# Kernel tuning notes

Hardware: AMD Instinct MI355X
Metric: run time of the kernel (lower is better)

## Reference

```python
import jax, jax.numpy as jnp
import numpy as np

B, S, H = 4, 2048, 768
NH, HD = 12, 64
E, TOPK, F = 8, 2, 3072

def rotate_half(x):
    x1, x2 = x[..., : x.shape[-1] // 2], x[..., x.shape[-1] // 2 :]
    return jnp.concatenate((-x2, x1), axis=-1)

def rope_cache(seq_len, dim, dtype=jnp.float32):
    inv_freq = 1.0 / (10000.0 ** (jnp.arange(0, dim, 2, dtype=jnp.float32) / dim))
    t = jnp.arange(seq_len, dtype=jnp.float32)
    freqs = jnp.einsum('i,j->ij', t, inv_freq)          # [S, dim/2]
    emb = jnp.concatenate((freqs, freqs), axis=-1)       # [S, dim]
    return jnp.cos(emb).astype(dtype), jnp.sin(emb).astype(dtype)

def rmsnorm(x, w):
    eps = jnp.finfo(x.dtype).eps
    var = jnp.mean(jnp.square(x), axis=-1, keepdims=True)
    return x * jax.lax.rsqrt(var + eps) * w

def setup_inputs() -> dict:
    key = jax.random.key(0)
    ks = jax.random.split(key, 9)
    s = lambda fan_in: 1.0 / np.sqrt(fan_in)
    return {
        'x': jax.random.normal(ks[0], (B, S, H), jnp.float32),
        'attention_mask': jnp.ones((B, S), jnp.int32),
        'qkv_w': jax.random.normal(ks[1], (H, 3 * H), jnp.float32) * s(H),
        'out_w': jax.random.normal(ks[2], (H, H), jnp.float32) * s(H),
        'gate_w': jax.random.normal(ks[3], (H, E), jnp.float32) * s(H),
        'w1': jax.random.normal(ks[4], (E, H, F), jnp.float32) * s(H),
        'w2': jax.random.normal(ks[5], (E, F, H), jnp.float32) * s(F),
        'norm1_w': jnp.ones((H,), jnp.float32),
        'norm2_w': jnp.ones((H,), jnp.float32),
    }

def reference(x, attention_mask, qkv_w, out_w, gate_w, w1, w2, norm1_w, norm2_w):
    b, seq, h = x.shape
    # ---- attention with manual RoPE ----
    qkv = (x @ qkv_w).reshape(b, seq, NH, 3 * HD).transpose(0, 2, 1, 3)  # [B,NH,S,3*HD]
    q, k, v = jnp.split(qkv, 3, axis=-1)
    cos, sin = rope_cache(seq, HD, x.dtype)  # [S,HD]
    cos = cos[None, None]; sin = sin[None, None]
    q = q * cos + rotate_half(q) * sin
    k = k * cos + rotate_half(k) * sin
    scores = jnp.einsum('bhqd,bhkd->bhqk', q, k) / jnp.sqrt(jnp.asarray(HD, x.dtype))
    mask = attention_mask[:, None, None, :]  # [B,1,1,S]
    scores = jnp.where(mask == 0, jnp.finfo(scores.dtype).min, scores)
    attn = jax.nn.softmax(scores, axis=-1)
    ctx = jnp.einsum('bhqk,bhkd->bhqd', attn, v)
    ctx = ctx.transpose(0, 2, 1, 3).reshape(b, seq, h)
    attn_out = ctx @ out_w
    x1 = rmsnorm(x + attn_out, norm1_w)
    # ---- MoE ----
    xf = x1.reshape(-1, h)                                # [T,H]
    T = xf.shape[0]
    router_logits = xf @ gate_w                           # [T,E]
    probs = jax.nn.softmax(router_logits.astype(jnp.float32), axis=-1)
    rw, sel = jax.lax.top_k(probs, TOPK)                  # [T,K]
    rw = rw / jnp.sum(rw, axis=-1, keepdims=True)
    # aux load-balancing loss
    counts = jnp.zeros((E,), jnp.float32).at[sel.reshape(-1)].add(1.0)
    f_i = counts / T
    P_i = probs.mean(axis=0)
    aux_loss = E * jnp.sum(f_i * P_i)
    # dense combine weights [T,E] (zero where expert not selected)
    cw = jnp.zeros((T, E), jnp.float32).at[jnp.arange(T)[:, None], sel].add(rw)
    # dense grouped expert compute (same math as gather/index_add dispatch)
    hmid = jax.nn.gelu(jnp.einsum('th,ehf->etf', xf, w1), approximate=False)
    yexp = jnp.einsum('etf,efh->eth', hmid, w2)           # [E,T,H]
    moe_out = jnp.einsum('eth,te->th', yexp, cw.astype(x.dtype))
    x2 = rmsnorm(x1 + moe_out.reshape(b, seq, h), norm2_w)
    return x2, aux_loss
```

## Files before the change

kernel.cpp:

```cpp
#include <hip/hip_runtime.h>
#include <hip/hip_bf16.h>
#include <math.h>

typedef __hip_bfloat16 bf16;
typedef __attribute__((ext_vector_type(8))) short bf16x8;
typedef __attribute__((ext_vector_type(4))) float f32x4;

#define B_ 4
#define S_ 2048
#define H_ 768
#define NH_ 12
#define HD_ 64
#define E_ 8
#define F_ 3072
#define T_ 8192

__device__ __forceinline__ unsigned f2bf(float x){
  unsigned u = __float_as_uint(x);
  return (u + 0x7FFFu + ((u >> 16) & 1u)) >> 16;
}

__device__ __forceinline__ float4 ldA4(const float* p){ return *reinterpret_cast<const float4*>(p); }

__device__ __forceinline__ float block_sum256(float v, float* red){
  int tid = threadIdx.x;
  red[tid] = v; __syncthreads();
  #pragma unroll
  for (int s = 128; s > 0; s >>= 1){
    if (tid < s) red[tid] += red[tid + s];
    __syncthreads();
  }
  float r = red[0];
  __syncthreads();
  return r;
}

__global__ __launch_bounds__(256) void gemm_f32_k(const float* __restrict__ A, const float* __restrict__ Bw,
                                                  float* __restrict__ C, int N, int K)
{
  __shared__ float As[16][132];
  __shared__ float Bs[16][132];
  const int tid = threadIdx.x;
  const int m0 = blockIdx.y * 128, n0 = blockIdx.x * 128;
  const int tm = tid >> 4, tn = tid & 15;
  const int am = tid >> 1, akq = (tid & 1) * 8;
  const int bk = tid >> 4, bnq = (tid & 15) * 8;
  float acc[8][8] = {};
  for (int k0 = 0; k0 < K; k0 += 16){
    float4 a0 = ldA4(&A[(size_t)(m0 + am) * K + k0 + akq]);
    float4 a1 = ldA4(&A[(size_t)(m0 + am) * K + k0 + akq + 4]);
    float4 b0 = ldA4(&Bw[(size_t)(k0 + bk) * N + n0 + bnq]);
    float4 b1 = ldA4(&Bw[(size_t)(k0 + bk) * N + n0 + bnq + 4]);
    As[akq+0][am] = a0.x; As[akq+1][am] = a0.y; As[akq+2][am] = a0.z; As[akq+3][am] = a0.w;
    As[akq+4][am] = a1.x; As[akq+5][am] = a1.y; As[akq+6][am] = a1.z; As[akq+7][am] = a1.w;
    *reinterpret_cast<float4*>(&Bs[bk][bnq])     = b0;
    *reinterpret_cast<float4*>(&Bs[bk][bnq + 4]) = b1;
    __syncthreads();
    #pragma unroll
    for (int kk = 0; kk < 16; ++kk){
      float4 av0 = *reinterpret_cast<const float4*>(&As[kk][tm*8]);
      float4 av1 = *reinterpret_cast<const float4*>(&As[kk][tm*8 + 4]);
      float4 bv0 = *reinterpret_cast<const float4*>(&Bs[kk][tn*8]);
      float4 bv1 = *reinterpret_cast<const float4*>(&Bs[kk][tn*8 + 4]);
      float a[8] = {av0.x,av0.y,av0.z,av0.w,av1.x,av1.y,av1.z,av1.w};
      float b[8] = {bv0.x,bv0.y,bv0.z,bv0.w,bv1.x,bv1.y,bv1.z,bv1.w};
      #pragma unroll
      for (int i = 0; i < 8; ++i)
        #pragma unroll
        for (int j = 0; j < 8; ++j)
          acc[i][j] += a[i]*b[j];
    }
    __syncthreads();
  }
  #pragma unroll
  for (int i = 0; i < 8; ++i){
    int row = m0 + tm*8 + i;
    float* dst = &C[(size_t)row * N + n0 + tn*8];
    *reinterpret_cast<float4*>(dst)     = make_float4(acc[i][0], acc[i][1], acc[i][2], acc[i][3]);
    *reinterpret_cast<float4*>(dst + 4) = make_float4(acc[i][4], acc[i][5], acc[i][6], acc[i][7]);
  }
}

__global__ __launch_bounds__(256) void rope_k(float* __restrict__ qkv)
{
  int idx = blockIdx.x * 256 + threadIdx.x;
  int j  = idx & 31;
  int hh = (idx >> 5) % NH_;
  int t  = idx / (32 * NH_);
  int s  = t & (S_ - 1);
  double invf = pow(10000.0, -(double)j / 32.0);
  float ph = (float)((double)s * invf);
  float sn, cs;
  sincosf(ph, &sn, &cs);
  float* base = qkv + (size_t)t * 2304 + hh * 192;
  float q0 = base[j],    q1 = base[32+j];
  base[j]    = q0*cs - q1*sn;
  base[32+j] = q1*cs + q0*sn;
  float k0 = base[64+j], k1 = base[96+j];
  base[64+j] = k0*cs - k1*sn;
  base[96+j] = k1*cs + k0*sn;
}

__global__ __launch_bounds__(256) void attn_mfma_k(const float* __restrict__ qkv,
                                                   const int* __restrict__ amask,
                                                   float* __restrict__ ctx)
{
  __shared__ __align__(16) short Kl[64*72];
  __shared__ __align__(16) short Vt[64*72];
  __shared__ __align__(16) short Pl[64*72];
  const int tid = threadIdx.x;
  const int qt = blockIdx.x & 31;
  const int hh = (blockIdx.x >> 5) % NH_;
  const int b  = blockIdx.x / (32 * NH_);
  const size_t tb = (size_t)b * S_;
  const int q0 = qt * 64;
  const int lane = tid & 63, w = tid >> 6;
  const int quad = lane >> 4, l15 = lane & 15;
  const int swl = (l15 & 12) << 1;

  bf16x8 qf[2];
  {
    const float* qrow = qkv + (tb + q0 + w*16 + l15) * 2304 + hh*192;
    #pragma unroll
    for (int ks = 0; ks < 2; ++ks){
      float4 f0 = ldA4(qrow + ks*32 + quad*8);
      float4 f1 = ldA4(qrow + ks*32 + quad*8 + 4);
      union { bf16x8 v; unsigned u[4]; } u;
      u.u[0] = f2bf(f0.x*0.125f) | (f2bf(f0.y*0.125f) << 16);
      u.u[1] = f2bf(f0.z*0.125f) | (f2bf(f0.w*0.125f) << 16);
      u.u[2] = f2bf(f1.x*0.125f) | (f2bf(f1.y*0.125f) << 16);
      u.u[3] = f2bf(f1.z*0.125f) | (f2bf(f1.w*0.125f) << 16);
      qf[ks] = u.v;
    }
  }

  f32x4 O[4];
  #pragma unroll
  for (int i = 0; i < 4; ++i) O[i] = (f32x4){0.f,0.f,0.f,0.f};
  float m_i[4] = {-3.0e38f,-3.0e38f,-3.0e38f,-3.0e38f};
  float l_i[4] = {0.f,0.f,0.f,0.f};

  for (int c = 0; c < 32; ++c){
    __syncthreads();
    #pragma unroll
    for (int i = 0; i < 2; ++i){
      int idx = i*256 + tid;
      int rp = idx >> 4;
      int c4 = (idx & 15) * 4;
      int r = rp * 2;
      const float* src = &qkv[(tb + c*64 + r) * 2304 + hh*192 + 64 + c4];
      float4 k0 = ldA4(src);
      float4 v0 = ldA4(src + 64);
      float4 k1 = ldA4(src + 2304);
      float4 v1 = ldA4(src + 2304 + 64);
      uint2 kw0, kw1;
      kw0.x = f2bf(k0.x) | (f2bf(k0.y) << 16); kw0.y = f2bf(k0.z) | (f2bf(k0.w) << 16);
      kw1.x = f2bf(k1.x) | (f2bf(k1.y) << 16); kw1.y = f2bf(k1.z) | (f2bf(k1.w) << 16);
      *reinterpret_cast<uint2*>(&Kl[ r   *72 + (c4 ^ (( r    & 12) << 1))]) = kw0;
      *reinterpret_cast<uint2*>(&Kl[(r+1)*72 + (c4 ^ (((r+1) & 12) << 1))]) = kw1;
      float vv0[4] = {v0.x,v0.y,v0.z,v0.w};
      float vv1[4] = {v1.x,v1.y,v1.z,v1.w};
      #pragma unroll
      for (int dd = 0; dd < 4; ++dd){
        int d = c4 + dd;
        unsigned pw = f2bf(vv0[dd]) | (f2bf(vv1[dd]) << 16);
        *reinterpret_cast<unsigned*>(&Vt[d*72 + (r ^ ((d & 12) << 1))]) = pw;
      }
    }
    __syncthreads();

    f32x4 sacc[4];
    #pragma unroll
    for (int ni = 0; ni < 4; ++ni) sacc[ni] = (f32x4){0.f,0.f,0.f,0.f};
    #pragma unroll
    for (int ks = 0; ks < 2; ++ks){
      #pragma unroll
      for (int ni = 0; ni < 4; ++ni){
        bf16x8 kf = *reinterpret_cast<const bf16x8*>(
            &Kl[(ni*16 + l15)*72 + ((quad*8 + ks*32) ^ swl)]);
        sacc[ni] = __builtin_amdgcn_mfma_f32_16x16x32_bf16(qf[ks], kf, sacc[ni], 0, 0, 0);
      }
    }

    #pragma unroll
    for (int ni = 0; ni < 4; ++ni){
      int mv = amask[b*S_ + c*64 + ni*16 + l15];
      if (mv == 0){
        sacc[ni][0] = -3.0e38f; sacc[ni][1] = -3.0e38f;
        sacc[ni][2] = -3.0e38f; sacc[ni][3] = -3.0e38f;
      }
    }
    float p[4][4];
    #pragma unroll
    for (int r = 0; r < 4; ++r){
      float v = fmaxf(fmaxf(sacc[0][r], sacc[1][r]), fmaxf(sacc[2][r], sacc[3][r]));
      #pragma unroll
      for (int o = 8; o > 0; o >>= 1) v = fmaxf(v, __shfl_xor(v, o, 64));
      float mn = fmaxf(m_i[r], v);
      float al = __expf(m_i[r] - mn);
      m_i[r] = mn;
      float ts = 0.f;
      #pragma unroll
      for (int ni = 0; ni < 4; ++ni){
        float e = __expf(sacc[ni][r] - mn);
        p[ni][r] = e; ts += e;
      }
      #pragma unroll
      for (int o = 8; o > 0; o >>= 1) ts += __shfl_xor(ts, o, 64);
      l_i[r] = l_i[r]*al + ts;
      #pragma unroll
      for (int nd = 0; nd < 4; ++nd) O[nd][r] *= al;
    }

    #pragma unroll
    for (int ni = 0; ni < 4; ++ni){
      int colp = (ni*16 + l15) ^ (quad << 3);
      #pragma unroll
      for (int r = 0; r < 4; ++r)
        Pl[(w*16 + quad*4 + r)*72 + colp] = (short)f2bf(p[ni][r]);
    }
    bf16x8 pa[2];
    #pragma unroll
    for (int ks = 0; ks < 2; ++ks)
      pa[ks] = *reinterpret_cast<const bf16x8*>(
          &Pl[(w*16 + l15)*72 + ((quad*8 + ks*32) ^ swl)]);

    #pragma unroll
    for (int ks = 0; ks < 2; ++ks){
      #pragma unroll
      for (int nd = 0; nd < 4; ++nd){
        bf16x8 vf = *reinterpret_cast<const bf16x8*>(
            &Vt[(nd*16 + l15)*72 + ((quad*8 + ks*32) ^ swl)]);
        O[nd] = __builtin_amdgcn_mfma_f32_16x16x32_bf16(pa[ks], vf, O[nd], 0, 0, 0);
      }
    }
  }

  #pragma unroll
  for (int r = 0; r < 4; ++r){
    float inv = 1.f / l_i[r];
    int row = q0 + w*16 + quad*4 + r;
    float* dst = &ctx[(tb + row)*H_ + hh*HD_ + l15];
    #pragma unroll
    for (int nd = 0; nd < 4; ++nd)
      dst[nd*16] = O[nd][r] * inv;
  }
}

__global__ __launch_bounds__(256) void norm1_k(const float* __restrict__ x, const float* __restrict__ ao,
                                               const float* __restrict__ w, float* __restrict__ x1)
{
  __shared__ float red[256];
  const int t = blockIdx.x, tid = threadIdx.x;
  float y[3]; float ss = 0.f;
  #pragma unroll
  for (int k = 0; k < 3; ++k){
    int i = tid + k*256;
    y[k] = x[(size_t)t*H_ + i] + ao[(size_t)t*H_ + i];
    ss += y[k]*y[k];
  }
  float tot = block_sum256(ss, red);
  float r = rsqrtf(tot / 768.f + 1.1920928955078125e-07f);
  #pragma unroll
  for (int k = 0; k < 3; ++k){
    int i = tid + k*256;
    x1[(size_t)t*H_ + i] = y[k] * r * w[i];
  }
}

__global__ __launch_bounds__(256) void router_k(const float* __restrict__ x1, const float* __restrict__ gw,
                                                float* __restrict__ rw, int* __restrict__ sel,
                                                float* __restrict__ Psum, int* __restrict__ cnt)
{
  __shared__ float lg[8];
  __shared__ float pr[8];
  const int t = blockIdx.x, tid = threadIdx.x;
  const int e = tid >> 5, l = tid & 31;
  const float* xr = x1 + (size_t)t * H_;
  float p = 0.f;
  for (int k = l; k < H_; k += 32) p += xr[k] * gw[k*E_ + e];
  #pragma unroll
  for (int o = 16; o > 0; o >>= 1) p += __shfl_xor(p, o, 32);
  if (l == 0) lg[e] = p;
  __syncthreads();
  if (tid == 0){
    float m = lg[0];
    #pragma unroll
    for (int i = 1; i < 8; ++i) m = fmaxf(m, lg[i]);
    float pv[8]; float s = 0.f;
    #pragma unroll
    for (int i = 0; i < 8; ++i){ pv[i] = expf(lg[i] - m); s += pv[i]; }
    float invs = 1.f / s;
    #pragma unroll
    for (int i = 0; i < 8; ++i){ pv[i] *= invs; pr[i] = pv[i]; }
    int i0 = 0;
    for (int i = 1; i < 8; ++i) if (pv[i] > pv[i0]) i0 = i;
    int i1 = -1;
    for (int i = 0; i < 8; ++i){ if (i == i0) continue; if (i1 < 0 || pv[i] > pv[i1]) i1 = i; }
    float w0 = pv[i0], w1 = pv[i1], si = 1.f / (w0 + w1);
    rw[2*t] = w0*si; rw[2*t+1] = w1*si;
    sel[2*t] = i0;   sel[2*t+1] = i1;
    atomicAdd(&cnt[i0], 1); atomicAdd(&cnt[i1], 1);
  }
  __syncthreads();
  if (tid < 8) atomicAdd(&Psum[tid], pr[tid]);
}

__global__ void offs_aux_k(const float* __restrict__ Psum, const int* __restrict__ cnt,
                           int* __restrict__ offs, float* __restrict__ aux_out)
{
  __shared__ float red[8];
  const int tid = threadIdx.x;
  if (tid == 0){
    int o = 0;
    for (int e = 0; e < 8; ++e){ offs[e] = o; o += cnt[e]; }
  }
  if (tid < 8) red[tid] = ((float)cnt[tid] / 8192.f) * (Psum[tid] / 8192.f);
  __syncthreads();
  if (tid == 0){
    float s = 0.f;
    for (int e = 0; e < 8; ++e) s += red[e];
    *aux_out = 8.f * s;
  }
}

__global__ __launch_bounds__(256) void scatter_k(const int* __restrict__ sel, const int* __restrict__ offs,
                                                 const float* __restrict__ rw,
                                                 int* __restrict__ cur, int* __restrict__ toka,
                                                 float* __restrict__ wgt)
{
  int t = blockIdx.x*256 + threadIdx.x;
  if (t >= T_) return;
  #pragma unroll
  for (int j = 0; j < 2; ++j){
    int e = sel[2*t + j];
    int pos = atomicAdd(&cur[e], 1);
    int a = offs[e] + pos;
    toka[a] = t;
    wgt[a] = rw[2*t + j];
  }
}

__global__ __launch_bounds__(256) void transpose_conv_k(const float* __restrict__ src,
                                                        unsigned short* __restrict__ dst,
                                                        int R, int C)
{
  __shared__ float T[32][33];
  const float* s = src + (size_t)blockIdx.z * R * C;
  unsigned short* d = dst + (size_t)blockIdx.z * R * C;
  int r0 = blockIdx.y*32, c0 = blockIdx.x*32;
  int t = threadIdx.x;
  int r = t >> 3, c4 = (t & 7) * 4;
  float4 v = ldA4(&s[(size_t)(r0+r)*C + c0 + c4]);
  T[r][c4+0]=v.x; T[r][c4+1]=v.y; T[r][c4+2]=v.z; T[r][c4+3]=v.w;
  __syncthreads();
  int c = t >> 3, r4 = (t & 7) * 4;
  ushort4 o;
  o.x = (unsigned short)f2bf(T[r4+0][c]);
  o.y = (unsigned short)f2bf(T[r4+1][c]);
  o.z = (unsigned short)f2bf(T[r4+2][c]);
  o.w = (unsigned short)f2bf(T[r4+3][c]);
  *reinterpret_cast<ushort4*>(&d[(size_t)(c0+c)*R + r0 + r4]) = o;
}

__global__ __launch_bounds__(256) void moe1_mfma_k(const float* __restrict__ X,
                                                   const unsigned short* __restrict__ Bt,
                                                   const int* __restrict__ offs,
                                                   const int* __restrict__ cnts,
                                                   const int* __restrict__ toka,
                                                   unsigned short* __restrict__ hmid)
{
  const int e = blockIdx.z;
  const int n_e = cnts[e];
  const int mt = blockIdx.y * 128;
  if (mt >= n_e) return;
  const int base = offs[e];
  const unsigned short* Bw = Bt + (size_t)e * (H_*F_);
  __shared__ __align__(16) short Al[8*129*8];
  __shared__ __align__(16) short Bl[8*129*8];
  const int tid = threadIdx.x;
  const int n0 = blockIdx.x * 128;
  int tokm[4];
  #pragma unroll
  for (int i = 0; i < 4; ++i){
    int m = (tid + i*256) >> 3;
    tokm[i] = toka[base + min(mt + m, n_e - 1)];
  }
  const int lane = tid & 63, w = tid >> 6;
  const int wr = w >> 1, wc = w & 1;
  const int quad = lane >> 4, l15 = lane & 15;
  f32x4 acc[4][4];
  #pragma unroll
  for (int a = 0; a < 4; ++a)
    #pragma unroll
    for (int b = 0; b < 4; ++b) acc[a][b] = (f32x4){0.f,0.f,0.f,0.f};

  for (int k0 = 0; k0 < H_; k0 += 64){
    __syncthreads();
    #pragma unroll
    for (int i = 0; i < 4; ++i){
      int c = tid + i*256;
      int m = c >> 3, kc = c & 7;
      const float* src = X + (size_t)tokm[i]*H_ + k0 + kc*8;
      float4 f0 = ldA4(src);
      float4 f1 = ldA4(src + 4);
      int4 pk;
      pk.x = (int)(f2bf(f0.x) | (f2bf(f0.y) << 16));
      pk.y = (int)(f2bf(f0.z) | (f2bf(f0.w) << 16));
      pk.z = (int)(f2bf(f1.x) | (f2bf(f1.y) << 16));
      pk.w = (int)(f2bf(f1.z) | (f2bf(f1.w) << 16));
      *reinterpret_cast<int4*>(&Al[(kc*129 + m)*8]) = pk;
      *reinterpret_cast<int4*>(&Bl[(kc*129 + m)*8]) =
        *reinterpret_cast<const int4*>(&Bw[(size_t)(n0 + m)*H_ + k0 + kc*8]);
    }
    __syncthreads();
    #pragma unroll
    for (int ks = 0; ks < 2; ++ks){
      bf16x8 af[4], bfr[4];
      #pragma unroll
      for (int mi = 0; mi < 4; ++mi)
        af[mi] = *reinterpret_cast<const bf16x8*>(&Al[((ks*4+quad)*129 + wr*64 + mi*16 + l15)*8]);
      #pragma unroll
      for (int ni = 0; ni < 4; ++ni)
        bfr[ni] = *reinterpret_cast<const bf16x8*>(&Bl[((ks*4+quad)*129 + wc*64 + ni*16 + l15)*8]);
      #pragma unroll
      for (int mi = 0; mi < 4; ++mi)
        #pragma unroll
        for (int ni = 0; ni < 4; ++ni)
          acc[mi][ni] = __builtin_amdgcn_mfma_f32_16x16x32_bf16(af[mi], bfr[ni], acc[mi][ni], 0, 0, 0);
    }
  }
  #pragma unroll
  for (int mi = 0; mi < 4; ++mi)
    #pragma unroll
    for (int r = 0; r < 4; ++r){
      int row = mt + wr*64 + mi*16 + quad*4 + r;
      if (row < n_e){
        unsigned short* dst = hmid + (size_t)(base + row)*F_ + n0 + wc*64 + l15;
        #pragma unroll
        for (int ni = 0; ni < 4; ++ni){
          float h = acc[mi][ni][r];
          float g = 0.5f * h * (1.f + erff(h * 0.70710678118654752f));
          dst[ni*16] = (unsigned short)f2bf(g);
        }
      }
    }
}

__global__ __launch_bounds__(256) void moe2_mfma_k(const unsigned short* __restrict__ Hm,
                                                   const unsigned short* __restrict__ Bt,
                                                   const int* __restrict__ offs,
                                                   const int* __restrict__ cnts,
                                                   const int* __restrict__ toka,
                                                   const float* __restrict__ wgt,
                                                   float* __restrict__ x1acc)
{
  const int e = blockIdx.z;
  const int n_e = cnts[e];
  const int mt = blockIdx.y * 128;
  if (mt >= n_e) return;
  const int base = offs[e];
  const unsigned short* Bw = Bt + (size_t)e * (H_*F_);
  __shared__ __align__(16) short Al[8*129*8];
  __shared__ __align__(16) short Bl[8*129*8];
  const int tid = threadIdx.x;
  const int n0 = blockIdx.x * 128;
  const int lane = tid & 63, w = tid >> 6;
  const int wr = w >> 1, wc = w & 1;
  const int quad = lane >> 4, l15 = lane & 15;
  f32x4 acc[4][4];
  #pragma unroll
  for (int a = 0; a < 4; ++a)
    #pragma unroll
    for (int b = 0; b < 4; ++b) acc[a][b] = (f32x4){0.f,0.f,0.f,0.f};

  for (int k0 = 0; k0 < F_; k0 += 64){
    __syncthreads();
    #pragma unroll
    for (int i = 0; i < 4; ++i){
      int c = tid + i*256;
      int m = c >> 3, kc = c & 7;
      int hrow = base + min(mt + m, n_e - 1);
      *reinterpret_cast<int4*>(&Al[(kc*129 + m)*8]) =
        *reinterpret_cast<const int4*>(&Hm[(size_t)hrow*F_ + k0 + kc*8]);
      *reinterpret_cast<int4*>(&Bl[(kc*129 + m)*8]) =
        *reinterpret_cast<const int4*>(&Bw[(size_t)(n0 + m)*F_ + k0 + kc*8]);
    }
    __syncthreads();
    #pragma unroll
    for (int ks = 0; ks < 2; ++ks){
      bf16x8 af[4], bfr[4];
      #pragma unroll
      for (int mi = 0; mi < 4; ++mi)
        af[mi] = *reinterpret_cast<const bf16x8*>(&Al[((ks*4+quad)*129 + wr*64 + mi*16 + l15)*8]);
      #pragma unroll
      for (int ni = 0; ni < 4; ++ni)
        bfr[ni] = *reinterpret_cast<const bf16x8*>(&Bl[((ks*4+quad)*129 + wc*64 + ni*16 + l15)*8]);
      #pragma unroll
      for (int mi = 0; mi < 4; ++mi)
        #pragma unroll
        for (int ni = 0; ni < 4; ++ni)
          acc[mi][ni] = __builtin_amdgcn_mfma_f32_16x16x32_bf16(af[mi], bfr[ni], acc[mi][ni], 0, 0, 0);
    }
  }
  #pragma unroll
  for (int mi = 0; mi < 4; ++mi)
    #pragma unroll
    for (int r = 0; r < 4; ++r){
      int row = mt + wr*64 + mi*16 + quad*4 + r;
      if (row < n_e){
        int tok = toka[base + row];
        float wg = wgt[base + row];
        float* dst = x1acc + (size_t)tok*H_ + n0 + wc*64 + l15;
        #pragma unroll
        for (int ni = 0; ni < 4; ++ni)
          atomicAdd(&dst[ni*16], acc[mi][ni][r] * wg);
      }
    }
}

__global__ __launch_bounds__(256) void norm2_k(const float* __restrict__ x1acc,
                                               const float* __restrict__ w, float* __restrict__ out)
{
  __shared__ float red[256];
  const int t = blockIdx.x, tid = threadIdx.x;
  const float* xr = x1acc + (size_t)t * H_;
  float y[3]; float ss = 0.f;
  #pragma unroll
  for (int k = 0; k < 3; ++k){
    int i = tid + k*256;
    y[k] = xr[i];
    ss += y[k]*y[k];
  }
  float tot = block_sum256(ss, red);
  float r = rsqrtf(tot / 768.f + 1.1920928955078125e-07f);
  #pragma unroll
  for (int k = 0; k < 3; ++k){
    int i = tid + k*256;
    out[(size_t)t*H_ + i] = y[k] * r * w[i];
  }
}

extern "C" void kernel_launch(void* const* d_in, const int* in_sizes, int n_in,
                              void* d_out, int out_size, void* d_ws, size_t ws_size,
                              hipStream_t stream)
{
  const float* x      = (const float*)d_in[0];
  const int*   amask  = (const int*)  d_in[1];
  const float* qkv_w  = (const float*)d_in[2];
  const float* out_w  = (const float*)d_in[3];
  const float* gate_w = (const float*)d_in[4];
  const float* w1     = (const float*)d_in[5];
  const float* w2     = (const float*)d_in[6];
  const float* n1w    = (const float*)d_in[7];
  const float* n2w    = (const float*)d_in[8];

  char* ws = (char*)d_ws;
  float* qkv  = (float*)(ws);
  float* ctx  = (float*)(ws + 75497472);
  float* attn = (float*)(ws);
  float* x1   = (float*)(ws + 100663296);
  unsigned short* hmid = (unsigned short*)(ws);
  unsigned short* w1T  = (unsigned short*)(ws + 125829120);
  unsigned short* w2T  = (unsigned short*)(ws + 125829120);
  float* rw   = (float*)(ws + 163577856);
  int*   sel  = (int*)  (ws + 163643392);
  int*   toka = (int*)  (ws + 163708928);
  float* wgt  = (float*)(ws + 163774464);
  float* Psum = (float*)(ws + 163840000);
  int*   cnt  = (int*)  (ws + 163840032);
  int*   cur  = (int*)  (ws + 163840064);
  int*   offs = (int*)  (ws + 163840096);

  float* out_x2  = (float*)d_out;
  float* out_aux = out_x2 + 6291456;

  hipMemsetAsync(ws + 163840000, 0, 128, stream);

  gemm_f32_k<<<dim3(18, 64), 256, 0, stream>>>(x, qkv_w, qkv, 2304, H_);
  rope_k<<<12288, 256, 0, stream>>>(qkv);
  attn_mfma_k<<<1536, 256, 0, stream>>>(qkv, amask, ctx);
  gemm_f32_k<<<dim3(6, 64), 256, 0, stream>>>(ctx, out_w, attn, H_, H_);
  norm1_k<<<T_, 256, 0, stream>>>(x, attn, n1w, x1);
  router_k<<<T_, 256, 0, stream>>>(x1, gate_w, rw, sel, Psum, cnt);
  offs_aux_k<<<1, 64, 0, stream>>>(Psum, cnt, offs, out_aux);
  scatter_k<<<32, 256, 0, stream>>>(sel, offs, rw, cur, toka, wgt);
  transpose_conv_k<<<dim3(96, 24, 8), 256, 0, stream>>>(w1, w1T, H_, F_);
  moe1_mfma_k<<<dim3(24, 64, 8), 256, 0, stream>>>(x1, w1T, offs, cnt, toka, hmid);
  transpose_conv_k<<<dim3(24, 96, 8), 256, 0, stream>>>(w2, w2T, F_, H_);
  moe2_mfma_k<<<dim3(6, 64, 8), 256, 0, stream>>>(hmid, w2T, offs, cnt, toka, wgt, x1);
  norm2_k<<<T_, 256, 0, stream>>>(x1, n2w, out_x2);
}
```

Before: 1.718 ms.

## Double-buffer fp32 GEMM shared tiles, pad B layout, and swizzle block order

After: 1.811 ms. 1.05x slower.

```diff
diff --git a/kernel.cpp b/kernel.cpp
--- a/kernel.cpp
+++ b/kernel.cpp
@@ -38,30 +38,51 @@
 __global__ __launch_bounds__(256) void gemm_f32_k(const float* __restrict__ A, const float* __restrict__ Bw,
                                                   float* __restrict__ C, int N, int K)
 {
-  __shared__ float As[16][132];
-  __shared__ float Bs[16][132];
+  __shared__ float As[2][16][132];
+  __shared__ float Bs[2][16][140];
   const int tid = threadIdx.x;
-  const int m0 = blockIdx.y * 128, n0 = blockIdx.x * 128;
+  const int gx = gridDim.x;
+  const int nwg = gx * gridDim.y;
+  const int bid = blockIdx.y * gx + blockIdx.x;
+  const int cpx = nwg >> 3;
+  const int swz = (bid & 7) * cpx + (bid >> 3);
+  const int m0 = (swz / gx) * 128, n0 = (swz % gx) * 128;
+
   const int tm = tid >> 4, tn = tid & 15;
   const int am = tid >> 1, akq = (tid & 1) * 8;
-  const int bk = tid >> 4, bnq = (tid & 15) * 8;
+  const int bk = tid >> 4, bo = tid & 15;
+  const int bg = bo * 8 + ((bo >> 2) << 2);
+  const int tg = tn * 8 + ((tn >> 2) << 2);
   float acc[8][8] = {};
-  for (int k0 = 0; k0 < K; k0 += 16){
-    float4 a0 = ldA4(&A[(size_t)(m0 + am) * K + k0 + akq]);
-    float4 a1 = ldA4(&A[(size_t)(m0 + am) * K + k0 + akq + 4]);
-    float4 b0 = ldA4(&Bw[(size_t)(k0 + bk) * N + n0 + bnq]);
-    float4 b1 = ldA4(&Bw[(size_t)(k0 + bk) * N + n0 + bnq + 4]);
-    As[akq+0][am] = a0.x; As[akq+1][am] = a0.y; As[akq+2][am] = a0.z; As[akq+3][am] = a0.w;
-    As[akq+4][am] = a1.x; As[akq+5][am] = a1.y; As[akq+6][am] = a1.z; As[akq+7][am] = a1.w;
-    *reinterpret_cast<float4*>(&Bs[bk][bnq])     = b0;
-    *reinterpret_cast<float4*>(&Bs[bk][bnq + 4]) = b1;
-    __syncthreads();
+
+  const float* Aptr = A + (size_t)(m0 + am) * K + akq;
+  const float* Bptr = Bw + (size_t)bk * N + n0 + bo * 8;
+
+  float4 a0 = ldA4(Aptr);
+  float4 a1 = ldA4(Aptr + 4);
+  float4 b0 = ldA4(Bptr);
+  float4 b1 = ldA4(Bptr + 4);
+  As[0][akq+0][am]=a0.x; As[0][akq+1][am]=a0.y; As[0][akq+2][am]=a0.z; As[0][akq+3][am]=a0.w;
+  As[0][akq+4][am]=a1.x; As[0][akq+5][am]=a1.y; As[0][akq+6][am]=a1.z; As[0][akq+7][am]=a1.w;
+  *reinterpret_cast<float4*>(&Bs[0][bk][bg])   = b0;
+  *reinterpret_cast<float4*>(&Bs[0][bk][bg+4]) = b1;
+
+  int buf = 0;
+  for (int k0 = 16; k0 <= K; k0 += 16){
+    const bool more = (k0 < K);
+    __syncthreads();
+    if (more){
+      a0 = ldA4(Aptr + k0);
+      a1 = ldA4(Aptr + k0 + 4);
+      b0 = ldA4(Bptr + (size_t)k0 * N);
+      b1 = ldA4(Bptr + (size_t)k0 * N + 4);
+    }
     #pragma unroll
     for (int kk = 0; kk < 16; ++kk){
-      float4 av0 = *reinterpret_cast<const float4*>(&As[kk][tm*8]);
-      float4 av1 = *reinterpret_cast<const float4*>(&As[kk][tm*8 + 4]);
-      float4 bv0 = *reinterpret_cast<const float4*>(&Bs[kk][tn*8]);
-      float4 bv1 = *reinterpret_cast<const float4*>(&Bs[kk][tn*8 + 4]);
+      float4 av0 = *reinterpret_cast<const float4*>(&As[buf][kk][tm*8]);
+      float4 av1 = *reinterpret_cast<const float4*>(&As[buf][kk][tm*8 + 4]);
+      float4 bv0 = *reinterpret_cast<const float4*>(&Bs[buf][kk][tg]);
+      float4 bv1 = *reinterpret_cast<const float4*>(&Bs[buf][kk][tg + 4]);
       float a[8] = {av0.x,av0.y,av0.z,av0.w,av1.x,av1.y,av1.z,av1.w};
       float b[8] = {bv0.x,bv0.y,bv0.z,bv0.w,bv1.x,bv1.y,bv1.z,bv1.w};
       #pragma unroll
@@ -70,7 +91,13 @@
         for (int j = 0; j < 8; ++j)
           acc[i][j] += a[i]*b[j];
     }
-    __syncthreads();
+    if (!more) break;
+    const int ob = buf ^ 1;
+    As[ob][akq+0][am]=a0.x; As[ob][akq+1][am]=a0.y; As[ob][akq+2][am]=a0.z; As[ob][akq+3][am]=a0.w;
+    As[ob][akq+4][am]=a1.x; As[ob][akq+5][am]=a1.y; As[ob][akq+6][am]=a1.z; As[ob][akq+7][am]=a1.w;
+    *reinterpret_cast<float4*>(&Bs[ob][bk][bg])   = b0;
+    *reinterpret_cast<float4*>(&Bs[ob][bk][bg+4]) = b1;
+    buf = ob;
   }
   #pragma unroll
   for (int i = 0; i < 8; ++i){
```

## Shrink FP32 GEMM tile to 64x128, add XCD block swizzle and LDS padding

Applied to the files above, without the earlier changes.

New measurement: 1.702 ms. No clear change (-0.9%).

```diff
diff --git a/kernel.cpp b/kernel.cpp
--- a/kernel.cpp
+++ b/kernel.cpp
@@ -38,34 +38,40 @@
 __global__ __launch_bounds__(256) void gemm_f32_k(const float* __restrict__ A, const float* __restrict__ Bw,
                                                   float* __restrict__ C, int N, int K)
 {
-  __shared__ float As[16][132];
-  __shared__ float Bs[16][132];
+  __shared__ float As[16][68];
+  __shared__ float Bs[16][140];
   const int tid = threadIdx.x;
-  const int m0 = blockIdx.y * 128, n0 = blockIdx.x * 128;
+  const int gx = gridDim.x;
+  const int nwg = gx * gridDim.y;
+  const int bid = blockIdx.y * gx + blockIdx.x;
+  const int cpx = nwg >> 3;
+  const int swz = (bid & 7) * cpx + (bid >> 3);
+  const int m0 = (swz / gx) * 64, n0 = (swz % gx) * 128;
+
   const int tm = tid >> 4, tn = tid & 15;
-  const int am = tid >> 1, akq = (tid & 1) * 8;
-  const int bk = tid >> 4, bnq = (tid & 15) * 8;
-  float acc[8][8] = {};
+  const int am = tid >> 2, akq = (tid & 3) * 4;
+  const int bk = tid >> 4, bo = tid & 15;
+  const int bg = bo * 8 + ((bo >> 2) << 2);
+  const int tg = tn * 8 + ((tn >> 2) << 2);
+  float acc[4][8] = {};
+
   for (int k0 = 0; k0 < K; k0 += 16){
-    float4 a0 = ldA4(&A[(size_t)(m0 + am) * K + k0 + akq]);
-    float4 a1 = ldA4(&A[(size_t)(m0 + am) * K + k0 + akq + 4]);
-    float4 b0 = ldA4(&Bw[(size_t)(k0 + bk) * N + n0 + bnq]);
-    float4 b1 = ldA4(&Bw[(size_t)(k0 + bk) * N + n0 + bnq + 4]);
-    As[akq+0][am] = a0.x; As[akq+1][am] = a0.y; As[akq+2][am] = a0.z; As[akq+3][am] = a0.w;
-    As[akq+4][am] = a1.x; As[akq+5][am] = a1.y; As[akq+6][am] = a1.z; As[akq+7][am] = a1.w;
-    *reinterpret_cast<float4*>(&Bs[bk][bnq])     = b0;
-    *reinterpret_cast<float4*>(&Bs[bk][bnq + 4]) = b1;
+    float4 av = ldA4(&A[(size_t)(m0 + am) * K + k0 + akq]);
+    float4 b0 = ldA4(&Bw[(size_t)(k0 + bk) * N + n0 + bo*8]);
+    float4 b1 = ldA4(&Bw[(size_t)(k0 + bk) * N + n0 + bo*8 + 4]);
+    As[akq+0][am] = av.x; As[akq+1][am] = av.y; As[akq+2][am] = av.z; As[akq+3][am] = av.w;
+    *reinterpret_cast<float4*>(&Bs[bk][bg])     = b0;
+    *reinterpret_cast<float4*>(&Bs[bk][bg + 4]) = b1;
     __syncthreads();
     #pragma unroll
     for (int kk = 0; kk < 16; ++kk){
-      float4 av0 = *reinterpret_cast<const float4*>(&As[kk][tm*8]);
-      float4 av1 = *reinterpret_cast<const float4*>(&As[kk][tm*8 + 4]);
-      float4 bv0 = *reinterpret_cast<const float4*>(&Bs[kk][tn*8]);
-      float4 bv1 = *reinterpret_cast<const float4*>(&Bs[kk][tn*8 + 4]);
-      float a[8] = {av0.x,av0.y,av0.z,av0.w,av1.x,av1.y,av1.z,av1.w};
+      float4 a4  = *reinterpret_cast<const float4*>(&As[kk][tm*4]);
+      float4 bv0 = *reinterpret_cast<const float4*>(&Bs[kk][tg]);
+      float4 bv1 = *reinterpret_cast<const float4*>(&Bs[kk][tg + 4]);
+      float a[4] = {a4.x,a4.y,a4.z,a4.w};
       float b[8] = {bv0.x,bv0.y,bv0.z,bv0.w,bv1.x,bv1.y,bv1.z,bv1.w};
       #pragma unroll
-      for (int i = 0; i < 8; ++i)
+      for (int i = 0; i < 4; ++i)
         #pragma unroll
         for (int j = 0; j < 8; ++j)
           acc[i][j] += a[i]*b[j];
@@ -73,8 +79,8 @@
     __syncthreads();
   }
   #pragma unroll
-  for (int i = 0; i < 8; ++i){
-    int row = m0 + tm*8 + i;
+  for (int i = 0; i < 4; ++i){
+    int row = m0 + tm*4 + i;
     float* dst = &C[(size_t)row * N + n0 + tn*8];
     *reinterpret_cast<float4*>(dst)     = make_float4(acc[i][0], acc[i][1], acc[i][2], acc[i][3]);
     *reinterpret_cast<float4*>(dst + 4) = make_float4(acc[i][4], acc[i][5], acc[i][6], acc[i][7]);
@@ -577,10 +583,10 @@
 
   hipMemsetAsync(ws + 163840000, 0, 128, stream);
 
-  gemm_f32_k<<<dim3(18, 64), 256, 0, stream>>>(x, qkv_w, qkv, 2304, H_);
+  gemm_f32_k<<<dim3(18, 128), 256, 0, stream>>>(x, qkv_w, qkv, 2304, H_);
   rope_k<<<12288, 256, 0, stream>>>(qkv);
   attn_mfma_k<<<1536, 256, 0, stream>>>(qkv, amask, ctx);
-  gemm_f32_k<<<dim3(6, 64), 256, 0, stream>>>(ctx, out_w, attn, H_, H_);
+  gemm_f32_k<<<dim3(6, 128), 256, 0, stream>>>(ctx, out_w, attn, H_, H_);
   norm1_k<<<T_, 256, 0, stream>>>(x, attn, n1w, x1);
   router_k<<<T_, 256, 0, stream>>>(x1, gate_w, rw, sel, Psum, cnt);
   offs_aux_k<<<1, 64, 0, stream>>>(Psum, cnt, offs, out_aux);
```
